# Kernel tuning notes

Hardware: AMD Instinct MI355X
Metric: run time of the kernel (lower is better)

Reference implementation:

```python
import jax, jax.numpy as jnp
import numpy as np

N_NODES = 50000


def _gcn_layer(x, src, dst, W, b, n_nodes):
    # PyG GCNConv: h = x @ W, add self-loops, sym-normalized scatter-add, + bias
    h = x @ W  # [N, Dout]
    loop = jnp.arange(n_nodes, dtype=src.dtype)
    src2 = jnp.concatenate([src, loop])
    dst2 = jnp.concatenate([dst, loop])
    ones = jnp.ones(src2.shape[0], dtype=x.dtype)
    deg = jax.ops.segment_sum(ones, dst2, num_segments=n_nodes)  # in-degree w/ self-loops
    dinv = jnp.where(deg > 0, jax.lax.rsqrt(deg), 0.0)
    norm = dinv[src2] * dinv[dst2]  # [E+N]
    msg = h[src2] * norm[:, None]   # gather + scale
    out = jax.ops.segment_sum(msg, dst2, num_segments=n_nodes)  # scatter-add
    return out + b


def setup_inputs() -> dict:
    key = jax.random.key(0)
    k1, k2, k3, k4 = jax.random.split(key, 4)
    x = jax.random.normal(k1, (N_NODES, 128), dtype=jnp.float32)
    edge_index = jax.random.randint(k2, (2, 500000), 0, N_NODES, dtype=jnp.int64)
    W1 = jax.random.normal(k3, (128, 128), dtype=jnp.float32) * (1.0 / np.sqrt(128))
    b1 = jnp.zeros((128,), dtype=jnp.float32)
    W2 = jax.random.normal(k4, (128, 64), dtype=jnp.float32) * (1.0 / np.sqrt(128))
    b2 = jnp.zeros((64,), dtype=jnp.float32)
    return {"x": x, "edge_index": edge_index, "W1": W1, "b1": b1, "W2": W2, "b2": b2}


def reference(x, edge_index, W1, b1, W2, b2):
    src, dst = edge_index[0], edge_index[1]
    n = x.shape[0]
    h = _gcn_layer(x, src, dst, W1, b1, n)
    h = jax.nn.relu(h)
    out = _gcn_layer(h, src, dst, W2, b2, n)
    return out
```

## Files before the change

### kernel.cpp

```cpp
#include <hip/hip_runtime.h>
#include <hip/hip_bf16.h>
#include <cstddef>


typedef __attribute__((ext_vector_type(8))) short short8;
typedef __attribute__((ext_vector_type(4))) float f32x4;
typedef unsigned long long u64;

__device__ inline unsigned short f2bf(float f) {
    __hip_bfloat16 b = __float2bfloat16(f);
    return *reinterpret_cast<unsigned short*>(&b);
}
__device__ inline float bf2f_lo(unsigned int u) {
    unsigned int v = u << 16;
    return *reinterpret_cast<float*>(&v);
}
__device__ inline float bf2f_hi(unsigned int u) {
    unsigned int v = u & 0xffff0000u;
    return *reinterpret_cast<float*>(&v);
}
__device__ inline u64 ld_acq64(u64* p) {
    return __hip_atomic_load(p, __ATOMIC_ACQUIRE, __HIP_MEMORY_SCOPE_AGENT);
}
__device__ inline void st_rel64(u64* p, u64 v) {
    __hip_atomic_store(p, v, __ATOMIC_RELEASE, __HIP_MEMORY_SCOPE_AGENT);
}

__global__ __launch_bounds__(256) void init_kernel(int* __restrict__ deg, int N,
                                                   const float* __restrict__ W1,
                                                   const float* __restrict__ W2,
                                                   unsigned short* __restrict__ W1f,
                                                   unsigned short* __restrict__ W2f,
                                                   u64* __restrict__ lb, int ZB) {
    int b = blockIdx.x;
    int tid = threadIdx.x;
    if (b < ZB) {
        int i = (b * 256 + tid) * 4;
        if (i + 3 < N) *(int4*)(deg + i) = make_int4(0, 0, 0, 0);
        else for (; i < N; i++) deg[i] = 0;
        return;
    }
    int idx = (b - ZB) * 256 + tid;
    if (idx < 64) lb[idx] = 0;
    if (idx < 3072) {
        const float* W;
        unsigned short* Wf;
        int n, oct, Nc;
        if (idx < 2048) { W = W1; Wf = W1f; Nc = 128; n = idx >> 4; oct = idx & 15; }
        else { W = W2; Wf = W2f; Nc = 64; int i2 = idx - 2048; n = i2 >> 4; oct = i2 & 15; }
        int k0 = oct * 8;
        int ks = k0 >> 5, quad = (k0 >> 3) & 3, ntg = n >> 4;
        short8 v;
        #pragma unroll
        for (int j = 0; j < 8; j++) v[j] = (short)f2bf(W[(k0 + j) * Nc + n]);
        int off = (((ntg * 4 + ks) * 64) + (n & 15) + 16 * quad) * 8;
        *(short8*)(Wf + off) = v;
    }
}

__global__ __launch_bounds__(256) void countgemm_kernel(
    const int* __restrict__ dst, int E,
    int* __restrict__ deg, unsigned short* __restrict__ rank,
    const float* __restrict__ x, const unsigned short* __restrict__ W1f,
    unsigned short* __restrict__ h1, int N, int CB) {

    int b = blockIdx.x;
    int tid = threadIdx.x;

    __shared__ unsigned short As[64 * 128];

    if (b < CB) {
        int i = (b * 256 + tid) * 4;
        if (i + 3 < E) {
            int4 d = *(const int4*)(dst + i);
            unsigned short r0 = (unsigned short)atomicAdd(&deg[d.x], 1);
            unsigned short r1 = (unsigned short)atomicAdd(&deg[d.y], 1);
            unsigned short r2 = (unsigned short)atomicAdd(&deg[d.z], 1);
            unsigned short r3 = (unsigned short)atomicAdd(&deg[d.w], 1);
            *(ushort4*)(rank + i) = make_ushort4(r0, r1, r2, r3);
        } else {
            for (; i < E; i++) rank[i] = (unsigned short)atomicAdd(&deg[dst[i]], 1);
        }
        return;
    }

    constexpr int K = 128, BN = 128;
    int lane = tid & 63;
    int w = tid >> 6;
    int row0 = (b - CB) * 64;

    short8 bfr[2][4];
    #pragma unroll
    for (int nl = 0; nl < 2; nl++)
        #pragma unroll
        for (int ks = 0; ks < 4; ks++)
            bfr[nl][ks] = *(const short8*)(W1f + ((((w * 2 + nl) * 4 + ks) * 64) + lane) * 8);

    #pragma unroll
    for (int it = 0; it < 8; it++) {
        int idx = it * 256 + tid;
        int row = idx >> 5, kq = idx & 31;
        int k0 = kq * 4;
        int ks = k0 >> 5, quad = (k0 >> 3) & 3, j0 = k0 & 7, mt = row >> 4;
        ushort4 o = make_ushort4(0, 0, 0, 0);
        int gr = row0 + row;
        if (gr < N) {
            float4 a = *(const float4*)(x + (size_t)gr * K + k0);
            o.x = f2bf(a.x); o.y = f2bf(a.y); o.z = f2bf(a.z); o.w = f2bf(a.w);
        }
        int off = (((mt * 4 + ks) * 64) + (row & 15) + 16 * quad) * 8 + j0;
        *(ushort4*)(As + off) = o;
    }
    __syncthreads();

    f32x4 acc[4][2];
    #pragma unroll
    for (int mt = 0; mt < 4; mt++)
        #pragma unroll
        for (int nl = 0; nl < 2; nl++) acc[mt][nl] = (f32x4){0.f, 0.f, 0.f, 0.f};

    #pragma unroll
    for (int ks = 0; ks < 4; ks++) {
        short8 af[4];
        #pragma unroll
        for (int mt = 0; mt < 4; mt++)
            af[mt] = *(const short8*)(As + (((mt * 4 + ks) * 64) + lane) * 8);
        #pragma unroll
        for (int mt = 0; mt < 4; mt++)
            #pragma unroll
            for (int nl = 0; nl < 2; nl++)
                acc[mt][nl] = __builtin_amdgcn_mfma_f32_16x16x32_bf16(
                    af[mt], bfr[nl][ks], acc[mt][nl], 0, 0, 0);
    }

    int col16 = lane & 15;
    int rowq = lane >> 4;
    #pragma unroll
    for (int mt = 0; mt < 4; mt++) {
        #pragma unroll
        for (int nl = 0; nl < 2; nl++) {
            int gc = (w * 2 + nl) * 16 + col16;
            #pragma unroll
            for (int r = 0; r < 4; r++) {
                int lr = mt * 16 + rowq * 4 + r;
                int gr = row0 + lr;
                if (gr < N) h1[(size_t)gr * BN + gc] = f2bf(acc[mt][nl][r]);
            }
        }
    }
}

__global__ __launch_bounds__(256) void scan_lb_kernel(const int* __restrict__ deg, int N,
                                                      u64* __restrict__ lb,
                                                      int* __restrict__ offs,
                                                      float* __restrict__ dinv) {
    __shared__ int ws[4];
    __shared__ int s_prefix;
    int tid = threadIdx.x;
    int sb = blockIdx.x;
    int SB = gridDim.x;
    int lane = tid & 63;
    int wv = tid >> 6;

    int i = sb * 1024 + tid * 4;
    int v0 = (i + 0 < N) ? deg[i + 0] : 0;
    int v1 = (i + 1 < N) ? deg[i + 1] : 0;
    int v2 = (i + 2 < N) ? deg[i + 2] : 0;
    int v3 = (i + 3 < N) ? deg[i + 3] : 0;
    int tsum = v0 + v1 + v2 + v3;
    int xs = tsum;
    #pragma unroll
    for (int off = 1; off < 64; off <<= 1) {
        int y = __shfl_up(xs, off, 64);
        if (lane >= off) xs += y;
    }
    if (lane == 63) ws[wv] = xs;
    __syncthreads();
    int wprefix = 0;
    #pragma unroll
    for (int w2 = 0; w2 < 4; w2++) wprefix += (w2 < wv) ? ws[w2] : 0;
    int chunk_total = ws[0] + ws[1] + ws[2] + ws[3];

    if (wv == 0) {
        if (lane == 0)
            st_rel64(&lb[sb], ((u64)(unsigned)chunk_total << 2) | 1ull);
        int contrib = 0;
        if (sb > 0) {
            int pred = sb - 1 - lane;
            for (;;) {
                u64 v = (pred >= 0) ? ld_acq64(&lb[pred]) : 2ull;
                int flag = (int)(v & 3);
                u64 ball2 = __ballot(flag == 2);
                u64 ball0 = __ballot(flag == 0);
                if (ball2 != 0) {
                    int L = __ffsll(ball2) - 1;
                    if ((ball0 & ((1ull << L) - 1)) == 0) {
                        contrib = (lane <= L) ? (int)(unsigned)(v >> 2) : 0;
                        break;
                    }
                }
                __builtin_amdgcn_s_sleep(1);
            }
            #pragma unroll
            for (int off = 32; off >= 1; off >>= 1)
                contrib += __shfl_xor(contrib, off, 64);
        }
        if (lane == 0) {
            st_rel64(&lb[sb], ((u64)(unsigned)(contrib + chunk_total) << 2) | 2ull);
            s_prefix = contrib;
        }
    }
    __syncthreads();

    int carry = s_prefix;
    int e0 = carry + wprefix + xs - tsum;
    int e1 = e0 + v0, e2 = e1 + v1, e3 = e2 + v2;
    if (i + 0 < N) { offs[i + 0] = e0; dinv[i + 0] = rsqrtf((float)(v0 + 1)); }
    if (i + 1 < N) { offs[i + 1] = e1; dinv[i + 1] = rsqrtf((float)(v1 + 1)); }
    if (i + 2 < N) { offs[i + 2] = e2; dinv[i + 2] = rsqrtf((float)(v2 + 1)); }
    if (i + 3 < N) { offs[i + 3] = e3; dinv[i + 3] = rsqrtf((float)(v3 + 1)); }
    if (sb == SB - 1 && tid == 0) offs[N] = carry + chunk_total;
}

__global__ __launch_bounds__(256) void fill_kernel(
    const int* __restrict__ src, const int* __restrict__ dst, int E,
    const int* __restrict__ offs, const unsigned short* __restrict__ rank,
    const float* __restrict__ dinv, int* __restrict__ csr,
    float* __restrict__ csrw) {
    int i = blockIdx.x * 256 + threadIdx.x;
    if (i < E) {
        int s = src[i];
        int d = dst[i];
        int pos = offs[d] + (int)rank[i];
        csr[pos] = s;
        csrw[pos] = dinv[s];
    }
}

__global__ __launch_bounds__(256) void aggmm_kernel(const unsigned short* __restrict__ h1,
                                                    const int* __restrict__ offs,
                                                    const int* __restrict__ csr,
                                                    const float* __restrict__ csrw,
                                                    const float* __restrict__ dinv,
                                                    const float* __restrict__ b1,
                                                    const unsigned short* __restrict__ W2f,
                                                    unsigned short* __restrict__ h2,
                                                    int n) {
    __shared__ unsigned short As[4 * 64 * 8];

    int tid = threadIdx.x;
    int t = tid & 63;
    int w = tid >> 6;
    int p = t >> 5;
    int t5 = t & 31;
    int nodebase = blockIdx.x * 16;
    int node0 = nodebase + w * 4;

    int ov = offs[min(node0 + min(t, 4), n)];
    int e0a[4], dega[4], nba[4], cidx[4];
    float cwv[4], dia[4];
    #pragma unroll
    for (int i = 0; i < 4; i++) {
        e0a[i] = __shfl(ov, i, 64);
        dega[i] = __shfl(ov, i + 1, 64) - e0a[i];
        nba[i] = min(dega[i], 64);
        int ce = e0a[i] + min(t, max(dega[i] - 1, 0));
        bool has = dega[i] > 0;
        cidx[i] = has ? csr[ce] : 0;
        cwv[i] = has ? csrw[ce] : 0.f;
        int node = node0 + i;
        dia[i] = (node < n) ? dinv[node] : 0.f;
    }

    short8 bw[4];
    #pragma unroll
    for (int ks = 0; ks < 4; ks++)
        bw[ks] = *(const short8*)(W2f + (((w * 4 + ks) * 64) + t) * 8);

    float4 bias = *(const float4*)(b1 + t5 * 4);

    float a[4][4];
    #pragma unroll
    for (int i = 0; i < 4; i++)
        #pragma unroll
        for (int k = 0; k < 4; k++) a[i][k] = 0.f;

    #pragma unroll
    for (int i = 0; i < 4; i++) {
        int node = node0 + i;
        if (node < n && p == 0) {
            uint2 su = *(const uint2*)(h1 + (size_t)node * 128 + t5 * 4);
            a[i][0] = bf2f_lo(su.x) * dia[i]; a[i][1] = bf2f_hi(su.x) * dia[i];
            a[i][2] = bf2f_lo(su.y) * dia[i]; a[i][3] = bf2f_hi(su.y) * dia[i];
        }
    }

    int itTop = (max(max(nba[0], nba[1]), max(nba[2], nba[3])) + 3) >> 2;
    for (int it = 0; it < itTop; ++it) {
        int base = it * 4;
        #pragma unroll
        for (int i = 0; i < 4; i++) {
            if (base < nba[i]) {
                #pragma unroll
                for (int j = 0; j < 2; j++) {
                    int ee = base + j * 2 + p;
                    int ec = min(ee, nba[i] - 1);
                    int s = __shfl(cidx[i], ec, 64);
                    float wv = __shfl(cwv[i], ec, 64);
                    wv = (ee < nba[i]) ? wv : 0.f;
                    uint2 hu = *(const uint2*)(h1 + (size_t)s * 128 + t5 * 4);
                    a[i][0] += bf2f_lo(hu.x) * wv; a[i][1] += bf2f_hi(hu.x) * wv;
                    a[i][2] += bf2f_lo(hu.y) * wv; a[i][3] += bf2f_hi(hu.y) * wv;
                }
            }
        }
    }
    #pragma unroll
    for (int i = 0; i < 4; i++) {
        int e1 = e0a[i] + dega[i];
        for (int eb = e0a[i] + 64; eb < e1; eb += 2) {
            int ee = eb + p;
            int ec = min(ee, e1 - 1);
            int s = csr[ec];
            float wv = (ee < e1) ? dinv[s] : 0.f;
            uint2 hu = *(const uint2*)(h1 + (size_t)s * 128 + t5 * 4);
            a[i][0] += bf2f_lo(hu.x) * wv; a[i][1] += bf2f_hi(hu.x) * wv;
            a[i][2] += bf2f_lo(hu.y) * wv; a[i][3] += bf2f_hi(hu.y) * wv;
        }
    }

    #pragma unroll
    for (int i = 0; i < 4; i++) {
        float a0 = a[i][0], a1 = a[i][1], a2 = a[i][2], a3 = a[i][3];
        a0 += __shfl_xor(a0, 32, 64);
        a1 += __shfl_xor(a1, 32, 64);
        a2 += __shfl_xor(a2, 32, 64);
        a3 += __shfl_xor(a3, 32, 64);
        if (p == 0) {
            a0 = fmaxf(a0 * dia[i] + bias.x, 0.f);
            a1 = fmaxf(a1 * dia[i] + bias.y, 0.f);
            a2 = fmaxf(a2 * dia[i] + bias.z, 0.f);
            a3 = fmaxf(a3 * dia[i] + bias.w, 0.f);
            int row16 = w * 4 + i;
            int k0 = t5 * 4;
            int ks = k0 >> 5, quad = (k0 >> 3) & 3, j0 = k0 & 7;
            ushort4 pk4 = make_ushort4(f2bf(a0), f2bf(a1), f2bf(a2), f2bf(a3));
            *(ushort4*)(As + ((ks * 64) + row16 + 16 * quad) * 8 + j0) = pk4;
        }
    }
    __syncthreads();

    f32x4 acc = (f32x4){0.f, 0.f, 0.f, 0.f};
    #pragma unroll
    for (int ks = 0; ks < 4; ks++) {
        short8 af = *(const short8*)(As + ((ks * 64) + t) * 8);
        acc = __builtin_amdgcn_mfma_f32_16x16x32_bf16(af, bw[ks], acc, 0, 0, 0);
    }

    int col = w * 16 + (t & 15);
    int rowq = t >> 4;
    #pragma unroll
    for (int r = 0; r < 4; r++) {
        int gr = nodebase + rowq * 4 + r;
        if (gr < n) h2[(size_t)gr * 64 + col] = f2bf(acc[r] * dinv[gr]);
    }
}

__global__ __launch_bounds__(256) void aggout_kernel(const unsigned short* __restrict__ h2,
                                                     const int* __restrict__ offs,
                                                     const int* __restrict__ csr,
                                                     const float* __restrict__ dinv,
                                                     const float* __restrict__ b2,
                                                     float* __restrict__ out, int n) {
    int tid = threadIdx.x;
    int t = tid & 63;
    int w = tid >> 6;
    int p = t >> 4;
    int t4 = t & 15;
    int node0 = blockIdx.x * 16 + w * 4;

    int ov = offs[min(node0 + min(t, 4), n)];
    int e0a[4], dega[4], nba[4], cidx[4];
    float dia[4];
    #pragma unroll
    for (int i = 0; i < 4; i++) {
        e0a[i] = __shfl(ov, i, 64);
        dega[i] = __shfl(ov, i + 1, 64) - e0a[i];
        nba[i] = min(dega[i], 64);
        int ce = e0a[i] + min(t, max(dega[i] - 1, 0));
        cidx[i] = (dega[i] > 0) ? csr[ce] : 0;
        int node = node0 + i;
        dia[i] = (node < n) ? dinv[node] : 0.f;
    }

    float a[4][4];
    #pragma unroll
    for (int i = 0; i < 4; i++)
        #pragma unroll
        for (int k = 0; k < 4; k++) a[i][k] = 0.f;

    #pragma unroll
    for (int i = 0; i < 4; i++) {
        int node = node0 + i;
        if (node < n && p == 0) {
            uint2 su = *(const uint2*)(h2 + (size_t)node * 64 + t4 * 4);
            a[i][0] = bf2f_lo(su.x); a[i][1] = bf2f_hi(su.x);
            a[i][2] = bf2f_lo(su.y); a[i][3] = bf2f_hi(su.y);
        }
    }

    int itTop = (max(max(nba[0], nba[1]), max(nba[2], nba[3])) + 3) >> 2;
    for (int it = 0; it < itTop; ++it) {
        int base = it * 4;
        #pragma unroll
        for (int i = 0; i < 4; i++) {
            if (base < nba[i]) {
                int ee = base + p;
                int ec = min(ee, nba[i] - 1);
                int s = __shfl(cidx[i], ec, 64);
                float wgt = (ee < nba[i]) ? 1.f : 0.f;
                uint2 hu = *(const uint2*)(h2 + (size_t)s * 64 + t4 * 4);
                a[i][0] += bf2f_lo(hu.x) * wgt; a[i][1] += bf2f_hi(hu.x) * wgt;
                a[i][2] += bf2f_lo(hu.y) * wgt; a[i][3] += bf2f_hi(hu.y) * wgt;
            }
        }
    }
    #pragma unroll
    for (int i = 0; i < 4; i++) {
        int e1 = e0a[i] + dega[i];
        for (int eb = e0a[i] + 64; eb < e1; eb += 4) {
            int ee = eb + p;
            int ec = min(ee, e1 - 1);
            int s = csr[ec];
            float wgt = (ee < e1) ? 1.f : 0.f;
            uint2 hu = *(const uint2*)(h2 + (size_t)s * 64 + t4 * 4);
            a[i][0] += bf2f_lo(hu.x) * wgt; a[i][1] += bf2f_hi(hu.x) * wgt;
            a[i][2] += bf2f_lo(hu.y) * wgt; a[i][3] += bf2f_hi(hu.y) * wgt;
        }
    }

    #pragma unroll
    for (int i = 0; i < 4; i++) {
        float a0 = a[i][0], a1 = a[i][1], a2 = a[i][2], a3 = a[i][3];
        a0 += __shfl_xor(a0, 16, 64); a1 += __shfl_xor(a1, 16, 64);
        a2 += __shfl_xor(a2, 16, 64); a3 += __shfl_xor(a3, 16, 64);
        a0 += __shfl_xor(a0, 32, 64); a1 += __shfl_xor(a1, 32, 64);
        a2 += __shfl_xor(a2, 32, 64); a3 += __shfl_xor(a3, 32, 64);
        int node = node0 + i;
        if (p == 0 && node < n) {
            float4 bb = *(const float4*)(b2 + t4 * 4);
            *(float4*)(out + (size_t)node * 64 + t4 * 4) =
                make_float4(a0 * dia[i] + bb.x, a1 * dia[i] + bb.y,
                            a2 * dia[i] + bb.z, a3 * dia[i] + bb.w);
        }
    }
}

extern "C" void kernel_launch(void* const* d_in, const int* in_sizes, int n_in,
                              void* d_out, int out_size, void* d_ws, size_t ws_size,
                              hipStream_t stream) {
    const float* x  = (const float*)d_in[0];
    const int*   ei = (const int*)d_in[1];
    const float* W1 = (const float*)d_in[2];
    const float* b1 = (const float*)d_in[3];
    const float* W2 = (const float*)d_in[4];
    const float* b2 = (const float*)d_in[5];

    const int N = in_sizes[0] / 128;
    const int E = in_sizes[1] / 2;
    const int* src = ei;
    const int* dst = ei + E;

    char* p = (char*)d_ws;
    auto alloc = [&](size_t bytes) {
        char* r = p;
        p += (bytes + 255) & ~(size_t)255;
        return r;
    };
    int*   degi  = (int*)  alloc((size_t)N * 4);
    float* dinv  = (float*)alloc((size_t)N * 4);
    int*   offs  = (int*)  alloc((size_t)(N + 1) * 4);
    u64*   lb    = (u64*)  alloc((size_t)64 * 8);
    unsigned short* rank = (unsigned short*)alloc((size_t)E * 2);
    int*            csr  = (int*)alloc((size_t)E * 4);
    float*          csrw = (float*)alloc((size_t)E * 4);
    unsigned short* W1f  = (unsigned short*)alloc((size_t)128 * 128 * 2);
    unsigned short* W2f  = (unsigned short*)alloc((size_t)64 * 128 * 2);
    unsigned short* h1   = (unsigned short*)alloc((size_t)N * 128 * 2);
    unsigned short* h2   = (unsigned short*)alloc((size_t)N * 64 * 2);
    float* out = (float*)d_out;

    const int GB = (N + 63) / 64;
    const int FB = (E + 255) / 256;
    const int SB = (N + 1023) / 1024;
    const int CB = (E / 4 + 255) / 256;
    const int ZB = (N + 1023) / 1024;

    init_kernel<<<ZB + 12, 256, 0, stream>>>(degi, N, W1, W2, W1f, W2f, lb, ZB);
    countgemm_kernel<<<CB + GB, 256, 0, stream>>>(dst, E, degi, rank, x, W1f, h1, N, CB);
    scan_lb_kernel<<<SB, 256, 0, stream>>>(degi, N, lb, offs, dinv);
    fill_kernel<<<FB, 256, 0, stream>>>(src, dst, E, offs, rank, dinv, csr, csrw);
    aggmm_kernel<<<(N + 15) / 16, 256, 0, stream>>>(h1, offs, csr, csrw, dinv, b1, W2f, h2, N);
    aggout_kernel<<<(N + 15) / 16, 256, 0, stream>>>(h2, offs, csr, dinv, b2, out, N);
}
```

Before: 190.6 us.

## Pre-scale h1 by source dinv in GEMM, drop csrw array, batch gathers

The layer-1 GEMM moves from the count kernel into the fill kernel, where dinv is already known, so each h1 row is pre-multiplied by its source node's dinv. This removes the per-edge csrw weight array and its writes and reads. The init kernel is replaced by hipMemsetAsync plus W conversion folded into the count kernel. The aggregation loops are restructured to issue several gathers before accumulating, to raise memory-level parallelism. Pre-scaling before bf16 rounding slightly changes numerics, and the unconditional batched gathers may issue redundant loads for low-degree nodes.

```diff
diff --git a/kernel.cpp b/kernel.cpp
--- a/kernel.cpp
+++ b/kernel.cpp
@@ -26,127 +26,45 @@
     __hip_atomic_store(p, v, __ATOMIC_RELEASE, __HIP_MEMORY_SCOPE_AGENT);
 }
 
-__global__ __launch_bounds__(256) void init_kernel(int* __restrict__ deg, int N,
-                                                   const float* __restrict__ W1,
-                                                   const float* __restrict__ W2,
-                                                   unsigned short* __restrict__ W1f,
-                                                   unsigned short* __restrict__ W2f,
-                                                   u64* __restrict__ lb, int ZB) {
+__global__ __launch_bounds__(256) void count_kernel(const int* __restrict__ dst, int E,
+                                                    int* __restrict__ deg,
+                                                    unsigned short* __restrict__ rank,
+                                                    const float* __restrict__ W1,
+                                                    const float* __restrict__ W2,
+                                                    unsigned short* __restrict__ W1f,
+                                                    unsigned short* __restrict__ W2f,
+                                                    u64* __restrict__ lb, int CB) {
     int b = blockIdx.x;
     int tid = threadIdx.x;
-    if (b < ZB) {
-        int i = (b * 256 + tid) * 4;
-        if (i + 3 < N) *(int4*)(deg + i) = make_int4(0, 0, 0, 0);
-        else for (; i < N; i++) deg[i] = 0;
+    if (b >= CB) {
+        int idx = (b - CB) * 256 + tid;
+        if (idx < 64) lb[idx] = 0;
+        if (idx < 3072) {
+            const float* W;
+            unsigned short* Wf;
+            int n, oct, Nc;
+            if (idx < 2048) { W = W1; Wf = W1f; Nc = 128; n = idx >> 4; oct = idx & 15; }
+            else { W = W2; Wf = W2f; Nc = 64; int i2 = idx - 2048; n = i2 >> 4; oct = i2 & 15; }
+            int k0 = oct * 8;
+            int ks = k0 >> 5, quad = (k0 >> 3) & 3, ntg = n >> 4;
+            short8 v;
+            #pragma unroll
+            for (int j = 0; j < 8; j++) v[j] = (short)f2bf(W[(k0 + j) * Nc + n]);
+            int off = (((ntg * 4 + ks) * 64) + (n & 15) + 16 * quad) * 8;
+            *(short8*)(Wf + off) = v;
+        }
         return;
     }
-    int idx = (b - ZB) * 256 + tid;
-    if (idx < 64) lb[idx] = 0;
-    if (idx < 3072) {
-        const float* W;
-        unsigned short* Wf;
-        int n, oct, Nc;
-        if (idx < 2048) { W = W1; Wf = W1f; Nc = 128; n = idx >> 4; oct = idx & 15; }
-        else { W = W2; Wf = W2f; Nc = 64; int i2 = idx - 2048; n = i2 >> 4; oct = i2 & 15; }
-        int k0 = oct * 8;
-        int ks = k0 >> 5, quad = (k0 >> 3) & 3, ntg = n >> 4;
-        short8 v;
-        #pragma unroll
-        for (int j = 0; j < 8; j++) v[j] = (short)f2bf(W[(k0 + j) * Nc + n]);
-        int off = (((ntg * 4 + ks) * 64) + (n & 15) + 16 * quad) * 8;
-        *(short8*)(Wf + off) = v;
-    }
-}
-
-__global__ __launch_bounds__(256) void countgemm_kernel(
-    const int* __restrict__ dst, int E,
-    int* __restrict__ deg, unsigned short* __restrict__ rank,
-    const float* __restrict__ x, const unsigned short* __restrict__ W1f,
-    unsigned short* __restrict__ h1, int N, int CB) {
-
-    int b = blockIdx.x;
-    int tid = threadIdx.x;
-
-    __shared__ unsigned short As[64 * 128];
-
-    if (b < CB) {
-        int i = (b * 256 + tid) * 4;
-        if (i + 3 < E) {
-            int4 d = *(const int4*)(dst + i);
-            unsigned short r0 = (unsigned short)atomicAdd(&deg[d.x], 1);
-            unsigned short r1 = (unsigned short)atomicAdd(&deg[d.y], 1);
-            unsigned short r2 = (unsigned short)atomicAdd(&deg[d.z], 1);
-            unsigned short r3 = (unsigned short)atomicAdd(&deg[d.w], 1);
-            *(ushort4*)(rank + i) = make_ushort4(r0, r1, r2, r3);
-        } else {
-            for (; i < E; i++) rank[i] = (unsigned short)atomicAdd(&deg[dst[i]], 1);
-        }
-        return;
-    }
-
-    constexpr int K = 128, BN = 128;
-    int lane = tid & 63;
-    int w = tid >> 6;
-    int row0 = (b - CB) * 64;
-
-    short8 bfr[2][4];
-    #pragma unroll
-    for (int nl = 0; nl < 2; nl++)
-        #pragma unroll
-        for (int ks = 0; ks < 4; ks++)
-            bfr[nl][ks] = *(const short8*)(W1f + ((((w * 2 + nl) * 4 + ks) * 64) + lane) * 8);
-
-    #pragma unroll
-    for (int it = 0; it < 8; it++) {
-        int idx = it * 256 + tid;
-        int row = idx >> 5, kq = idx & 31;
-        int k0 = kq * 4;
-        int ks = k0 >> 5, quad = (k0 >> 3) & 3, j0 = k0 & 7, mt = row >> 4;
-        ushort4 o = make_ushort4(0, 0, 0, 0);
-        int gr = row0 + row;
-        if (gr < N) {
-            float4 a = *(const float4*)(x + (size_t)gr * K + k0);
-            o.x = f2bf(a.x); o.y = f2bf(a.y); o.z = f2bf(a.z); o.w = f2bf(a.w);
-        }
-        int off = (((mt * 4 + ks) * 64) + (row & 15) + 16 * quad) * 8 + j0;
-        *(ushort4*)(As + off) = o;
-    }
-    __syncthreads();
-
-    f32x4 acc[4][2];
-    #pragma unroll
-    for (int mt = 0; mt < 4; mt++)
-        #pragma unroll
-        for (int nl = 0; nl < 2; nl++) acc[mt][nl] = (f32x4){0.f, 0.f, 0.f, 0.f};
-
-    #pragma unroll
-    for (int ks = 0; ks < 4; ks++) {
-        short8 af[4];
-        #pragma unroll
-        for (int mt = 0; mt < 4; mt++)
-            af[mt] = *(const short8*)(As + (((mt * 4 + ks) * 64) + lane) * 8);
-        #pragma unroll
-        for (int mt = 0; mt < 4; mt++)
-            #pragma unroll
-            for (int nl = 0; nl < 2; nl++)
-                acc[mt][nl] = __builtin_amdgcn_mfma_f32_16x16x32_bf16(
-                    af[mt], bfr[nl][ks], acc[mt][nl], 0, 0, 0);
-    }
-
-    int col16 = lane & 15;
-    int rowq = lane >> 4;
-    #pragma unroll
-    for (int mt = 0; mt < 4; mt++) {
-        #pragma unroll
-        for (int nl = 0; nl < 2; nl++) {
-            int gc = (w * 2 + nl) * 16 + col16;
-            #pragma unroll
-            for (int r = 0; r < 4; r++) {
-                int lr = mt * 16 + rowq * 4 + r;
-                int gr = row0 + lr;
-                if (gr < N) h1[(size_t)gr * BN + gc] = f2bf(acc[mt][nl][r]);
-            }
-        }
+    int i = (b * 256 + tid) * 4;
+    if (i + 3 < E) {
+        int4 d = *(const int4*)(dst + i);
+        unsigned short r0 = (unsigned short)atomicAdd(&deg[d.x], 1);
+        unsigned short r1 = (unsigned short)atomicAdd(&deg[d.y], 1);
+        unsigned short r2 = (unsigned short)atomicAdd(&deg[d.z], 1);
+        unsigned short r3 = (unsigned short)atomicAdd(&deg[d.w], 1);
+        *(ushort4*)(rank + i) = make_ushort4(r0, r1, r2, r3);
+    } else {
+        for (; i < E; i++) rank[i] = (unsigned short)atomicAdd(&deg[dst[i]], 1);
     }
 }
 
@@ -222,25 +140,105 @@
     if (sb == SB - 1 && tid == 0) offs[N] = carry + chunk_total;
 }
 
-__global__ __launch_bounds__(256) void fill_kernel(
+__global__ __launch_bounds__(256) void fillgemm_kernel(
+    const float* __restrict__ x, const unsigned short* __restrict__ W1f,
+    unsigned short* __restrict__ h1, int N,
     const int* __restrict__ src, const int* __restrict__ dst, int E,
     const int* __restrict__ offs, const unsigned short* __restrict__ rank,
-    const float* __restrict__ dinv, int* __restrict__ csr,
-    float* __restrict__ csrw) {
-    int i = blockIdx.x * 256 + threadIdx.x;
-    if (i < E) {
-        int s = src[i];
-        int d = dst[i];
-        int pos = offs[d] + (int)rank[i];
-        csr[pos] = s;
-        csrw[pos] = dinv[s];
+    const float* __restrict__ dinv, int* __restrict__ csr) {
+
+    const int FB = (E + 255) / 256;
+    int b = blockIdx.x;
+    int tid = threadIdx.x;
+
+    __shared__ unsigned short As[64 * 128];
+    __shared__ float sdinv[64];
+
+    if (b < FB) {
+        int i = b * 256 + tid;
+        if (i < E) {
+            int s = src[i];
+            int d = dst[i];
+            int pos = offs[d] + (int)rank[i];
+            csr[pos] = s;
+        }
+        return;
+    }
+
+    constexpr int K = 128, BN = 128;
+    int lane = tid & 63;
+    int w = tid >> 6;
+    int row0 = (b - FB) * 64;
+
+    if (tid < 64) {
+        int gr = row0 + tid;
+        sdinv[tid] = (gr < N) ? dinv[gr] : 0.f;
+    }
+
+    short8 bfr[2][4];
+    #pragma unroll
+    for (int nl = 0; nl < 2; nl++)
+        #pragma unroll
+        for (int ks = 0; ks < 4; ks++)
+            bfr[nl][ks] = *(const short8*)(W1f + ((((w * 2 + nl) * 4 + ks) * 64) + lane) * 8);
+
+    #pragma unroll
+    for (int it = 0; it < 8; it++) {
+        int idx = it * 256 + tid;
+        int row = idx >> 5, kq = idx & 31;
+        int k0 = kq * 4;
+        int ks = k0 >> 5, quad = (k0 >> 3) & 3, j0 = k0 & 7, mt = row >> 4;
+        ushort4 o = make_ushort4(0, 0, 0, 0);
+        int gr = row0 + row;
+        if (gr < N) {
+            float4 a = *(const float4*)(x + (size_t)gr * K + k0);
+            o.x = f2bf(a.x); o.y = f2bf(a.y); o.z = f2bf(a.z); o.w = f2bf(a.w);
+        }
+        int off = (((mt * 4 + ks) * 64) + (row & 15) + 16 * quad) * 8 + j0;
+        *(ushort4*)(As + off) = o;
+    }
+    __syncthreads();
+
+    f32x4 acc[4][2];
+    #pragma unroll
+    for (int mt = 0; mt < 4; mt++)
+        #pragma unroll
+        for (int nl = 0; nl < 2; nl++) acc[mt][nl] = (f32x4){0.f, 0.f, 0.f, 0.f};
+
+    #pragma unroll
+    for (int ks = 0; ks < 4; ks++) {
+        short8 af[4];
+        #pragma unroll
+        for (int mt = 0; mt < 4; mt++)
+            af[mt] = *(const short8*)(As + (((mt * 4 + ks) * 64) + lane) * 8);
+        #pragma unroll
+        for (int mt = 0; mt < 4; mt++)
+            #pragma unroll
+            for (int nl = 0; nl < 2; nl++)
+                acc[mt][nl] = __builtin_amdgcn_mfma_f32_16x16x32_bf16(
+                    af[mt], bfr[nl][ks], acc[mt][nl], 0, 0, 0);
+    }
+
+    int col16 = lane & 15;
+    int rowq = lane >> 4;
+    #pragma unroll
+    for (int mt = 0; mt < 4; mt++) {
+        #pragma unroll
+        for (int nl = 0; nl < 2; nl++) {
+            int gc = (w * 2 + nl) * 16 + col16;
+            #pragma unroll
+            for (int r = 0; r < 4; r++) {
+                int lr = mt * 16 + rowq * 4 + r;
+                int gr = row0 + lr;
+                if (gr < N) h1[(size_t)gr * BN + gc] = f2bf(acc[mt][nl][r] * sdinv[lr]);
+            }
+        }
     }
 }
 
 __global__ __launch_bounds__(256) void aggmm_kernel(const unsigned short* __restrict__ h1,
                                                     const int* __restrict__ offs,
                                                     const int* __restrict__ csr,
-                                                    const float* __restrict__ csrw,
                                                     const float* __restrict__ dinv,
                                                     const float* __restrict__ b1,
                                                     const unsigned short* __restrict__ W2f,
@@ -258,16 +256,14 @@
 
     int ov = offs[min(node0 + min(t, 4), n)];
     int e0a[4], dega[4], nba[4], cidx[4];
-    float cwv[4], dia[4];
+    float dia[4];
     #pragma unroll
     for (int i = 0; i < 4; i++) {
         e0a[i] = __shfl(ov, i, 64);
         dega[i] = __shfl(ov, i + 1, 64) - e0a[i];
         nba[i] = min(dega[i], 64);
         int ce = e0a[i] + min(t, max(dega[i] - 1, 0));
-        bool has = dega[i] > 0;
-        cidx[i] = has ? csr[ce] : 0;
-        cwv[i] = has ? csrw[ce] : 0.f;
+        cidx[i] = (dega[i] > 0) ? csr[ce] : 0;
         int node = node0 + i;
         dia[i] = (node < n) ? dinv[node] : 0.f;
     }
@@ -290,42 +286,51 @@
         int node = node0 + i;
         if (node < n && p == 0) {
             uint2 su = *(const uint2*)(h1 + (size_t)node * 128 + t5 * 4);
-            a[i][0] = bf2f_lo(su.x) * dia[i]; a[i][1] = bf2f_hi(su.x) * dia[i];
-            a[i][2] = bf2f_lo(su.y) * dia[i]; a[i][3] = bf2f_hi(su.y) * dia[i];
+            a[i][0] = bf2f_lo(su.x); a[i][1] = bf2f_hi(su.x);
+            a[i][2] = bf2f_lo(su.y); a[i][3] = bf2f_hi(su.y);
         }
     }
 
     int itTop = (max(max(nba[0], nba[1]), max(nba[2], nba[3])) + 3) >> 2;
     for (int it = 0; it < itTop; ++it) {
         int base = it * 4;
+        uint2 hu[4][2];
+        float wv[4][2];
         #pragma unroll
         for (int i = 0; i < 4; i++) {
-            if (base < nba[i]) {
-                #pragma unroll
-                for (int j = 0; j < 2; j++) {
-                    int ee = base + j * 2 + p;
-                    int ec = min(ee, nba[i] - 1);
-                    int s = __shfl(cidx[i], ec, 64);
-                    float wv = __shfl(cwv[i], ec, 64);
-                    wv = (ee < nba[i]) ? wv : 0.f;
-                    uint2 hu = *(const uint2*)(h1 + (size_t)s * 128 + t5 * 4);
-                    a[i][0] += bf2f_lo(hu.x) * wv; a[i][1] += bf2f_hi(hu.x) * wv;
-                    a[i][2] += bf2f_lo(hu.y) * wv; a[i][3] += bf2f_hi(hu.y) * wv;
-                }
-            }
-        }
+            #pragma unroll
+            for (int j = 0; j < 2; j++) {
+                int ee = base + j * 2 + p;
+                int ec = min(ee, nba[i] - 1);
+                int s = __shfl(cidx[i], ec, 64);
+                wv[i][j] = (ee < nba[i]) ? 1.f : 0.f;
+                hu[i][j] = *(const uint2*)(h1 + (size_t)s * 128 + t5 * 4);
+            }
+        }
+        #pragma unroll
+        for (int i = 0; i < 4; i++)
+            #pragma unroll
+            for (int j = 0; j < 2; j++) {
+                a[i][0] += bf2f_lo(hu[i][j].x) * wv[i][j];
+                a[i][1] += bf2f_hi(hu[i][j].x) * wv[i][j];
+                a[i][2] += bf2f_lo(hu[i][j].y) * wv[i][j];
+                a[i][3] += bf2f_hi(hu[i][j].y) * wv[i][j];
+            }
     }
     #pragma unroll
     for (int i = 0; i < 4; i++) {
         int e1 = e0a[i] + dega[i];
-        for (int eb = e0a[i] + 64; eb < e1; eb += 2) {
-            int ee = eb + p;
-            int ec = min(ee, e1 - 1);
-            int s = csr[ec];
-            float wv = (ee < e1) ? dinv[s] : 0.f;
-            uint2 hu = *(const uint2*)(h1 + (size_t)s * 128 + t5 * 4);
-            a[i][0] += bf2f_lo(hu.x) * wv; a[i][1] += bf2f_hi(hu.x) * wv;
-            a[i][2] += bf2f_lo(hu.y) * wv; a[i][3] += bf2f_hi(hu.y) * wv;
+        for (int eb = e0a[i] + 64; eb < e1; eb += 8) {
+            #pragma unroll
+            for (int j = 0; j < 4; j++) {
+                int ee = eb + j * 2 + p;
+                int ec = min(ee, e1 - 1);
+                int s = csr[ec];
+                float wgt = (ee < e1) ? 1.f : 0.f;
+                uint2 hu = *(const uint2*)(h1 + (size_t)s * 128 + t5 * 4);
+                a[i][0] += bf2f_lo(hu.x) * wgt; a[i][1] += bf2f_hi(hu.x) * wgt;
+                a[i][2] += bf2f_lo(hu.y) * wgt; a[i][3] += bf2f_hi(hu.y) * wgt;
+            }
         }
     }
 
@@ -409,33 +414,46 @@
         }
     }
 
-    int itTop = (max(max(nba[0], nba[1]), max(nba[2], nba[3])) + 3) >> 2;
+    int itTop = (max(max(nba[0], nba[1]), max(nba[2], nba[3])) + 7) >> 3;
     for (int it = 0; it < itTop; ++it) {
-        int base = it * 4;
+        int base = it * 8;
+        uint2 hu[4][2];
+        float wv[4][2];
         #pragma unroll
         for (int i = 0; i < 4; i++) {
-            if (base < nba[i]) {
-                int ee = base + p;
+            #pragma unroll
+            for (int j = 0; j < 2; j++) {
+                int ee = base + j * 4 + p;
                 int ec = min(ee, nba[i] - 1);
                 int s = __shfl(cidx[i], ec, 64);
-                float wgt = (ee < nba[i]) ? 1.f : 0.f;
+                wv[i][j] = (ee < nba[i]) ? 1.f : 0.f;
+                hu[i][j] = *(const uint2*)(h2 + (size_t)s * 64 + t4 * 4);
+            }
+        }
+        #pragma unroll
+        for (int i = 0; i < 4; i++)
+            #pragma unroll
+            for (int j = 0; j < 2; j++) {
+                a[i][0] += bf2f_lo(hu[i][j].x) * wv[i][j];
+                a[i][1] += bf2f_hi(hu[i][j].x) * wv[i][j];
+                a[i][2] += bf2f_lo(hu[i][j].y) * wv[i][j];
+                a[i][3] += bf2f_hi(hu[i][j].y) * wv[i][j];
+            }
+    }
+    #pragma unroll
+    for (int i = 0; i < 4; i++) {
+        int e1 = e0a[i] + dega[i];
+        for (int eb = e0a[i] + 64; eb < e1; eb += 8) {
+            #pragma unroll
+            for (int j = 0; j < 2; j++) {
+                int ee = eb + j * 4 + p;
+                int ec = min(ee, e1 - 1);
+                int s = csr[ec];
+                float wgt = (ee < e1) ? 1.f : 0.f;
                 uint2 hu = *(const uint2*)(h2 + (size_t)s * 64 + t4 * 4);
                 a[i][0] += bf2f_lo(hu.x) * wgt; a[i][1] += bf2f_hi(hu.x) * wgt;
                 a[i][2] += bf2f_lo(hu.y) * wgt; a[i][3] += bf2f_hi(hu.y) * wgt;
             }
-        }
-    }
-    #pragma unroll
-    for (int i = 0; i < 4; i++) {
-        int e1 = e0a[i] + dega[i];
-        for (int eb = e0a[i] + 64; eb < e1; eb += 4) {
-            int ee = eb + p;
-            int ec = min(ee, e1 - 1);
-            int s = csr[ec];
-            float wgt = (ee < e1) ? 1.f : 0.f;
-            uint2 hu = *(const uint2*)(h2 + (size_t)s * 64 + t4 * 4);
-            a[i][0] += bf2f_lo(hu.x) * wgt; a[i][1] += bf2f_hi(hu.x) * wgt;
-            a[i][2] += bf2f_lo(hu.y) * wgt; a[i][3] += bf2f_hi(hu.y) * wgt;
         }
     }
 
@@ -483,7 +501,6 @@
     u64*   lb    = (u64*)  alloc((size_t)64 * 8);
     unsigned short* rank = (unsigned short*)alloc((size_t)E * 2);
     int*            csr  = (int*)alloc((size_t)E * 4);
-    float*          csrw = (float*)alloc((size_t)E * 4);
     unsigned short* W1f  = (unsigned short*)alloc((size_t)128 * 128 * 2);
     unsigned short* W2f  = (unsigned short*)alloc((size_t)64 * 128 * 2);
     unsigned short* h1   = (unsigned short*)alloc((size_t)N * 128 * 2);
@@ -494,12 +511,13 @@
     const int FB = (E + 255) / 256;
     const int SB = (N + 1023) / 1024;
     const int CB = (E / 4 + 255) / 256;
-    const int ZB = (N + 1023) / 1024;
-
-    init_kernel<<<ZB + 12, 256, 0, stream>>>(degi, N, W1, W2, W1f, W2f, lb, ZB);
-    countgemm_kernel<<<CB + GB, 256, 0, stream>>>(dst, E, degi, rank, x, W1f, h1, N, CB);
+
+    hipMemsetAsync(degi, 0, (size_t)N * 4, stream);
+    count_kernel<<<CB + 12, 256, 0, stream>>>(dst, E, degi, rank,
+                                              W1, W2, W1f, W2f, lb, CB);
     scan_lb_kernel<<<SB, 256, 0, stream>>>(degi, N, lb, offs, dinv);
-    fill_kernel<<<FB, 256, 0, stream>>>(src, dst, E, offs, rank, dinv, csr, csrw);
-    aggmm_kernel<<<(N + 15) / 16, 256, 0, stream>>>(h1, offs, csr, csrw, dinv, b1, W2f, h2, N);
+    fillgemm_kernel<<<FB + GB, 256, 0, stream>>>(x, W1f, h1, N, src, dst, E,
+                                                 offs, rank, dinv, csr);
+    aggmm_kernel<<<(N + 15) / 16, 256, 0, stream>>>(h1, offs, csr, dinv, b1, W2f, h2, N);
     aggout_kernel<<<(N + 15) / 16, 256, 0, stream>>>(h2, offs, csr, dinv, b2, out, N);
 }
```

Measured after the change: 174.9 us. 1.09x faster.
